# Optimization experiments

Measured on AMD Instinct MI355X. Metric: run time of the kernel, lower is better.

The kernel has to match this reference:

```python
import jax, jax.numpy as jnp
import numpy as np

N = 50000          # nodes
E = 800000         # edges (avg degree 16)
DIN = 128          # d_input
H = 8              # heads per layer
D = 16             # per-head hidden dim
HID = H * D        # 128
ALPHA = 0.2        # LeakyReLU negative slope in GAT attention
BN_EPS = 1e-5


def _xavier(key, shape):
    fan_in, fan_out = shape[0], shape[-1]
    lim = np.sqrt(6.0 / (fan_in + fan_out)).astype(np.float32)
    return jax.random.uniform(key, shape, jnp.float32, -lim, lim)


def setup_inputs() -> dict:
    key = jax.random.key(0)
    ks = jax.random.split(key, 8)
    x = jax.random.normal(ks[0], (N, DIN), jnp.float32)
    edge_idx = jax.random.randint(ks[1], (2, E), 0, N)
    W1 = _xavier(ks[2], (DIN, HID))
    a1 = _xavier(ks[3], (H, 2 * D))
    W2 = _xavier(ks[4], (HID, HID))
    a2 = _xavier(ks[5], (H, 2 * D))
    W3 = _xavier(ks[6], (HID, HID))
    a3 = _xavier(ks[7], (H, 2 * D))
    ones = jnp.ones((HID,), jnp.float32)
    zeros = jnp.zeros((HID,), jnp.float32)
    return {"x": x, "edge_idx": edge_idx,
            "W1": W1, "a1": a1, "W2": W2, "a2": a2, "W3": W3, "a3": a3,
            "g1": ones, "b1": zeros, "g2": ones, "b2": zeros, "g3": ones, "b3": zeros}


def _leaky(x):
    return jnp.where(x >= 0, x, ALPHA * x)


def _gat_layer(x, src, dst, W, a):
    # x: [N, Fin]; W: [Fin, H*D]; a: [H, 2D]
    h = (x @ W).reshape(-1, H, D)                       # [N, H, D]
    e_src = jnp.einsum('nhd,hd->nh', h, a[:, :D])       # a^T part for source node
    e_dst = jnp.einsum('nhd,hd->nh', h, a[:, D:])       # a^T part for destination node
    e = _leaky(e_src[src] + e_dst[dst])                 # [E, H]
    m = jax.ops.segment_max(e, dst, num_segments=N)     # per-dst stable softmax max
    m = jnp.where(jnp.isfinite(m), m, 0.0)              # empty segments -> 0
    w = jnp.exp(e - m[dst])                             # [E, H]
    den = jax.ops.segment_sum(w, dst, num_segments=N)   # [N, H]
    agg = jax.ops.segment_sum(h[src] * w[:, :, None], dst, num_segments=N)  # [N, H, D]
    out = agg / (den[:, :, None] + 1e-16)
    return out.reshape(-1, HID)                         # concat heads


def _bn(x, g, b):
    # BatchNorm1d training-mode math over the node axis
    mu = x.mean(axis=0)
    var = x.var(axis=0)
    return g * (x - mu) * jax.lax.rsqrt(var + BN_EPS) + b


def reference(x, edge_idx, W1, a1, W2, a2, W3, a3, g1, b1, g2, b2, g3, b3):
    src, dst = edge_idx[0], edge_idx[1]
    h1 = jax.nn.elu(_bn(_gat_layer(x, src, dst, W1, a1), g1, b1))
    h2 = jax.nn.elu(_bn(_gat_layer(h1, src, dst, W2, a2), g2, b2))
    h3_in = h1 + h2  # skip connection
    return _bn(_gat_layer(h3_in, src, dst, W3, a3), g3, b3)
```

## Files before the change

kernel.cpp:

```cpp
#include <hip/hip_runtime.h>
#include <hip/hip_bf16.h>
#include <hip/hip_fp16.h>
#include <cstddef>

#define NNODES 50000
#define NEDGES 800000
#define HID 128
#define NHEAD 8
#define AGG_NB (NNODES / 16)
#define NSLICE 64
#define SLAYER (NSLICE * 512)

#define NBUCK 196
#define BCH 2048
#define BIN_NB ((NEDGES + BCH - 1) / BCH)

typedef __attribute__((ext_vector_type(4))) float floatx4;
typedef _Float16 __attribute__((ext_vector_type(8))) half8;
typedef _Float16 __attribute__((ext_vector_type(2))) half2v;

static inline size_t align_up(size_t x, size_t a) { return (x + a - 1) & ~(a - 1); }

__device__ inline float fexp2(float x) {
#if __has_builtin(__builtin_amdgcn_exp2f)
    return __builtin_amdgcn_exp2f(x);
#else
    return __expf(x * 0.69314718055994531f);
#endif
}

__device__ inline unsigned short f2h(float f) {
    return __builtin_bit_cast(unsigned short, (_Float16)f);
}

__global__ __launch_bounds__(256) void init_kernel(const float* __restrict__ W1,
                                                   const float* __restrict__ W2,
                                                   const float* __restrict__ W3,
                                                   unsigned short* __restrict__ Wt,
                                                   int* __restrict__ zeroA, int nA,
                                                   float* __restrict__ zeroB, int nB) {
    int b = blockIdx.x;
    int t = threadIdx.x;
    if (b < 192) {
        int layer = b >> 6;
        const float* W = (layer == 0) ? W1 : ((layer == 1) ? W2 : W3);
        int idx = (b & 63) * 256 + t;
        int n = idx & 127;
        int k = idx >> 7;
        Wt[layer * 16384 + n * 128 + k] = f2h(W[idx]);
    } else {
        int nb = gridDim.x - 192;
        int bb = b - 192;
        for (int i = bb * 256 + t; i < nA; i += nb * 256) zeroA[i] = 0;
        for (int i = bb * 256 + t; i < nB; i += nb * 256) zeroB[i] = 0.f;
    }
}

__global__ __launch_bounds__(256) void bin_count_kernel(const int* __restrict__ edge,
                                                        int* __restrict__ bucketCnt) {
    __shared__ int h[NBUCK];
    int t = threadIdx.x;
    if (t < NBUCK) h[t] = 0;
    __syncthreads();
    for (int i = blockIdx.x * 256 + t; i < NEDGES; i += gridDim.x * 256)
        atomicAdd(&h[edge[NEDGES + i] >> 8], 1);
    __syncthreads();
    if (t < NBUCK && h[t]) atomicAdd(&bucketCnt[t], h[t]);
}

__global__ __launch_bounds__(256) void bucket_scan_kernel(const int* __restrict__ bucketCnt,
                                                          int* __restrict__ bucketBase) {
    __shared__ int sA[256];
    int t = threadIdx.x;
    int v = (t < NBUCK) ? bucketCnt[t] : 0;
    sA[t] = v;
    __syncthreads();
    for (int off = 1; off < 256; off <<= 1) {
        int x = (t >= off) ? sA[t - off] : 0;
        __syncthreads();
        sA[t] += x;
        __syncthreads();
    }
    if (t < NBUCK) bucketBase[t] = sA[t] - v;
    if (t == 0) bucketBase[NBUCK] = NEDGES;
}

__global__ __launch_bounds__(256) void bin_scatter_kernel(const int* __restrict__ edge,
                                                          const int* __restrict__ bucketBase,
                                                          int* __restrict__ bucketCursor,
                                                          unsigned int* __restrict__ binned) {
    __shared__ int sA[256];
    __shared__ int hcnt[NBUCK];
    __shared__ int hbase[NBUCK];
    __shared__ int gbase[NBUCK];
    __shared__ unsigned int sEnt[BCH];
    __shared__ unsigned char sBk[BCH];
    int t = threadIdx.x;
    int e0 = blockIdx.x * BCH;
    int nv = NEDGES - e0;
    if (nv > BCH) nv = BCH;

    if (t < NBUCK) hcnt[t] = 0;
    __syncthreads();

    int myB[8];
    int myR[8];
    unsigned int myP[8];
    #pragma unroll
    for (int j = 0; j < 8; ++j) {
        int idx = j * 256 + t;
        myB[j] = -1;
        if (idx < nv) {
            int s = edge[e0 + idx];
            int d = edge[NEDGES + e0 + idx];
            int bk = d >> 8;
            myB[j] = bk;
            myP[j] = (unsigned)s | ((unsigned)(d & 255) << 16);
            myR[j] = atomicAdd(&hcnt[bk], 1);
        }
    }
    __syncthreads();
    int hc = (t < NBUCK) ? hcnt[t] : 0;
    sA[t] = hc;
    __syncthreads();
    for (int off = 1; off < 256; off <<= 1) {
        int x = (t >= off) ? sA[t - off] : 0;
        __syncthreads();
        sA[t] += x;
        __syncthreads();
    }
    if (t < NBUCK) {
        hbase[t] = sA[t] - hc;
        gbase[t] = bucketBase[t] + atomicAdd(&bucketCursor[t], hc);
    }
    __syncthreads();
    #pragma unroll
    for (int j = 0; j < 8; ++j) {
        if (myB[j] >= 0) {
            int p = hbase[myB[j]] + myR[j];
            sEnt[p] = myP[j];
            sBk[p] = (unsigned char)myB[j];
        }
    }
    __syncthreads();
    #pragma unroll
    for (int j = 0; j < 8; ++j) {
        int i = j * 256 + t;
        if (i < nv) {
            int bk = sBk[i];
            binned[gbase[bk] + (i - hbase[bk])] = sEnt[i];
        }
    }
}

__global__ __launch_bounds__(256) void fine_csr_kernel(const int* __restrict__ bucketCnt,
                                                       const int* __restrict__ bucketBase,
                                                       const unsigned int* __restrict__ binned,
                                                       int* __restrict__ offs,
                                                       int* __restrict__ csr) {
    __shared__ int sA[256];
    __shared__ int sB[256];
    int t = threadIdx.x;
    int b = blockIdx.x;
    int cntb = bucketCnt[b];
    int base = bucketBase[b];
    sB[t] = 0;
    __syncthreads();
    for (int i = t; i < cntb; i += 256)
        atomicAdd(&sB[(binned[base + i] >> 16) & 255], 1);
    __syncthreads();
    int nc = sB[t];
    sA[t] = nc;
    __syncthreads();
    for (int off = 1; off < 256; off <<= 1) {
        int x = (t >= off) ? sA[t - off] : 0;
        __syncthreads();
        sA[t] += x;
        __syncthreads();
    }
    int nodeBase = base + sA[t] - nc;
    int gid = b * 256 + t;
    if (gid < NNODES) offs[gid] = nodeBase;
    if (b == NBUCK - 1 && t == 0) offs[NNODES] = NEDGES;
    sB[t] = nodeBase;
    __syncthreads();
    for (int i = t; i < cntb; i += 256) {
        unsigned e = binned[base + i];
        int pos = atomicAdd(&sB[(e >> 16) & 255], 1);
        csr[pos] = (int)(e & 0xFFFFu);
    }
}

__global__ __launch_bounds__(256) void bn_finalize_kernel(const float* __restrict__ statsPart,
                                                          const float* __restrict__ g,
                                                          const float* __restrict__ b,
                                                          float* __restrict__ ssv) {
    __shared__ float sm[256];
    int t = threadIdx.x;
    const float* base = statsPart + (t & 127) + ((t >> 7) << 7);
    float s = 0.f;
    #pragma unroll 8
    for (int k = 0; k < NSLICE; ++k) s += base[k * 512];
    sm[t] = s;
    __syncthreads();
    if (t < 128) {
        float mu = sm[t] / (float)NNODES;
        float var = sm[128 + t] / (float)NNODES - mu * mu;
        float rstd = rsqrtf(var + 1e-5f);
        float scale = g[t] * rstd;
        ssv[t] = scale;
        ssv[128 + t] = b[t] - mu * scale;
    }
}

#define GROWS 32
#define TSTRIDE 76
#define LOG2E 1.4426950408889634f
__global__ __launch_bounds__(256, 4) void gemm_kernel(const float* __restrict__ Xin,
                                                      const float* __restrict__ skip,
                                                      const float* __restrict__ ssv,
                                                      const unsigned short* __restrict__ Wt,
                                                      const float* __restrict__ a,
                                                      float* __restrict__ Hw,
                                                      unsigned short* __restrict__ Hb,
                                                      float* __restrict__ esrc,
                                                      float* __restrict__ edst,
                                                      int mode) {
    __shared__ unsigned short As[4 * 16 * TSTRIDE];
    int tid = threadIdx.x;
    int wv = tid >> 6;
    int lane = tid & 63;
    int l15 = lane & 15;
    int quad = lane >> 4;
    int whalf = wv & 1;
    int rowBase = blockIdx.x * GROWS + (wv >> 1) * 16;
    int gr = rowBase + l15;
    bool valid = gr < NNODES;

    float4 va[8];
    if (valid) {
        const float* xr = Xin + (size_t)gr * HID + quad * 8;
        #pragma unroll
        for (int c = 0; c < 4; ++c) {
            va[2 * c]     = *(const float4*)(xr + c * 32);
            va[2 * c + 1] = *(const float4*)(xr + c * 32 + 4);
        }
    } else {
        #pragma unroll
        for (int j = 0; j < 8; ++j) va[j] = make_float4(0.f, 0.f, 0.f, 0.f);
    }
    float4 vs[8];
    if (mode == 2 && valid) {
        const float* sr = skip + (size_t)gr * HID + quad * 8;
        #pragma unroll
        for (int c = 0; c < 4; ++c) {
            vs[2 * c]     = *(const float4*)(sr + c * 32);
            vs[2 * c + 1] = *(const float4*)(sr + c * 32 + 4);
        }
    }

    half8 bf[2][4];
    {
        const unsigned short* wb = Wt + ((whalf * 4) * 16 + l15) * 128 + quad * 8;
        #pragma unroll
        for (int c = 0; c < 4; ++c) bf[0][c] = *(const half8*)(wb + c * 32);
    }

    if (mode >= 1 && valid) {
        #pragma unroll
        for (int c = 0; c < 4; ++c) {
            #pragma unroll
            for (int hh = 0; hh < 2; ++hh) {
                int ch = quad * 8 + c * 32 + hh * 4;
                float4 sc = *(const float4*)(ssv + ch);
                float4 sh = *(const float4*)(ssv + 128 + ch);
                float4 v = va[2 * c + hh];
                v.x = sc.x * v.x + sh.x;
                v.y = sc.y * v.y + sh.y;
                v.z = sc.z * v.z + sh.z;
                v.w = sc.w * v.w + sh.w;
                v.x = (v.x > 0.f) ? v.x : expm1f(v.x);
                v.y = (v.y > 0.f) ? v.y : expm1f(v.y);
                v.z = (v.z > 0.f) ? v.z : expm1f(v.z);
                v.w = (v.w > 0.f) ? v.w : expm1f(v.w);
                if (mode == 2) {
                    float4 s = vs[2 * c + hh];
                    v.x += s.x; v.y += s.y; v.z += s.z; v.w += s.w;
                }
                va[2 * c + hh] = v;
            }
        }
        if (mode == 1 && whalf == 0) {
            float* hw = Hw + (size_t)gr * HID + quad * 8;
            #pragma unroll
            for (int c = 0; c < 4; ++c) {
                *(float4*)(hw + c * 32)     = va[2 * c];
                *(float4*)(hw + c * 32 + 4) = va[2 * c + 1];
            }
        }
    }
    half8 af[4];
    #pragma unroll
    for (int c = 0; c < 4; ++c) {
        uint4 pk;
        pk.x = __builtin_bit_cast(unsigned int, __builtin_amdgcn_cvt_pkrtz(va[2*c].x,   va[2*c].y));
        pk.y = __builtin_bit_cast(unsigned int, __builtin_amdgcn_cvt_pkrtz(va[2*c].z,   va[2*c].w));
        pk.z = __builtin_bit_cast(unsigned int, __builtin_amdgcn_cvt_pkrtz(va[2*c+1].x, va[2*c+1].y));
        pk.w = __builtin_bit_cast(unsigned int, __builtin_amdgcn_cvt_pkrtz(va[2*c+1].z, va[2*c+1].w));
        af[c] = __builtin_bit_cast(half8, pk);
    }

    floatx4 acc[4];
    #pragma unroll
    for (int hb = 0; hb < 4; ++hb) {
        if (hb < 3) {
            const unsigned short* wn = Wt + ((whalf * 4 + hb + 1) * 16 + l15) * 128 + quad * 8;
            #pragma unroll
            for (int c = 0; c < 4; ++c) bf[(hb + 1) & 1][c] = *(const half8*)(wn + c * 32);
        }
        acc[hb] = (floatx4){0.f, 0.f, 0.f, 0.f};
        #pragma unroll
        for (int c = 0; c < 4; ++c)
            acc[hb] = __builtin_amdgcn_mfma_f32_16x16x32_f16(af[c], bf[hb & 1][c], acc[hb], 0, 0, 0);
    }

    unsigned short* ws = &As[wv * 16 * TSTRIDE];
    #pragma unroll
    for (int hb = 0; hb < 4; ++hb) {
        #pragma unroll
        for (int reg = 0; reg < 4; ++reg)
            ws[(quad * 4 + reg) * TSTRIDE + hb * 16 + l15] = f2h(acc[hb][reg]);
    }

    {
        int rloc = lane >> 2;
        int cpart = lane & 3;
        int grow = rowBase + rloc;
        const unsigned short* rrow = &ws[rloc * TSTRIDE + cpart * 16];
        uint4 u0 = *(const uint4*)(rrow);
        uint4 u1 = *(const uint4*)(rrow + 8);
        if (grow < NNODES) {
            int chb = whalf * 64 + cpart * 16;
            uint4* dst = (uint4*)(Hb + (size_t)grow * HID + chb);
            dst[0] = u0;
            dst[1] = u1;
            float f[16];
            {
                unsigned int* pu = (unsigned int*)&u0;
                #pragma unroll
                for (int j = 0; j < 4; ++j) {
                    half2v hv = __builtin_bit_cast(half2v, pu[j]);
                    f[2 * j]     = (float)hv[0];
                    f[2 * j + 1] = (float)hv[1];
                }
                pu = (unsigned int*)&u1;
                #pragma unroll
                for (int j = 0; j < 4; ++j) {
                    half2v hv = __builtin_bit_cast(half2v, pu[j]);
                    f[8 + 2 * j]     = (float)hv[0];
                    f[8 + 2 * j + 1] = (float)hv[1];
                }
            }
            int head = whalf * 4 + cpart;
            float es = 0.f, ev = 0.f;
            #pragma unroll
            for (int j = 0; j < 16; ++j) {
                es += f[j] * a[head * 32 + j];
                ev += f[j] * a[head * 32 + 16 + j];
            }
            esrc[grow * NHEAD + head] = es * LOG2E;
            edst[grow * NHEAD + head] = ev * LOG2E;
        }
    }
}

__global__ __launch_bounds__(256) void aggregate_kernel(const int* __restrict__ offs,
                                                        const int* __restrict__ csr,
                                                        const float* __restrict__ esrc,
                                                        const float* __restrict__ edst,
                                                        const unsigned int* __restrict__ Hb,
                                                        float* __restrict__ out,
                                                        float* __restrict__ statsPart) {
    int tid = threadIdx.x;
    int wv = tid >> 6;
    int lane = tid & 63;
    int grp = lane >> 4;
    int sub = lane & 15;
    int head = sub >> 1;
    int n = blockIdx.x * 16 + wv * 4 + grp;
    int beg = offs[n], end = offs[n + 1];
    float ed = edst[n * NHEAD + head];
    float acc[8];
    #pragma unroll
    for (int q = 0; q < 8; ++q) acc[q] = 0.f;
    float den = 0.f;
    for (int i = beg; i < end; i += 4) {
        int ss[4];
        #pragma unroll
        for (int j = 0; j < 4; ++j)
            ss[j] = csr[min(i + j, end - 1)];
        float ee[4];
        uint4 hh[4];
        #pragma unroll
        for (int j = 0; j < 4; ++j)
            ee[j] = esrc[(unsigned)ss[j] * 8u + (unsigned)head];
        #pragma unroll
        for (int j = 0; j < 4; ++j)
            hh[j] = *(const uint4*)(Hb + (unsigned)ss[j] * 64u + (unsigned)sub * 4u);
        #pragma unroll
        for (int j = 0; j < 4; ++j) {
            float e = ee[j] + ed;
            e = fmaxf(e, 0.2f * e);
            float w = fexp2(e);
            w = (i + j < end) ? w : 0.f;
            den += w;
            half2v h0 = __builtin_bit_cast(half2v, hh[j].x);
            half2v h1 = __builtin_bit_cast(half2v, hh[j].y);
            half2v h2 = __builtin_bit_cast(half2v, hh[j].z);
            half2v h3 = __builtin_bit_cast(half2v, hh[j].w);
            acc[0] += w * (float)h0[0];
            acc[1] += w * (float)h0[1];
            acc[2] += w * (float)h1[0];
            acc[3] += w * (float)h1[1];
            acc[4] += w * (float)h2[0];
            acc[5] += w * (float)h2[1];
            acc[6] += w * (float)h3[0];
            acc[7] += w * (float)h3[1];
        }
    }
    float inv = 1.f / (den + 1e-16f);
    float4 o0 = make_float4(acc[0] * inv, acc[1] * inv, acc[2] * inv, acc[3] * inv);
    float4 o1 = make_float4(acc[4] * inv, acc[5] * inv, acc[6] * inv, acc[7] * inv);
    float* orow = out + (size_t)n * HID + sub * 8;
    *(float4*)orow = o0;
    *(float4*)(orow + 4) = o1;

    __shared__ float sm[16 * 136];
    float* srow = &sm[(wv * 4 + grp) * 136 + sub * 8];
    *(float4*)srow = o0;
    *(float4*)(srow + 4) = o1;
    __syncthreads();
    if (tid < 128) {
        float s = 0.f, s2 = 0.f;
        #pragma unroll
        for (int rr = 0; rr < 16; ++rr) {
            float v = sm[rr * 136 + tid];
            s += v;
            s2 += v * v;
        }
        float* slice = statsPart + (blockIdx.x & (NSLICE - 1)) * 512;
        atomicAdd(&slice[tid], s);
        atomicAdd(&slice[128 + tid], s2);
    }
}

__global__ __launch_bounds__(256) void final_apply_kernel(const float* __restrict__ X,
                                                          const float* __restrict__ ssv,
                                                          float* __restrict__ out) {
    __shared__ float ssm[256];
    int tid = threadIdx.x;
    ssm[tid] = ssv[tid];
    __syncthreads();
    int total4 = NNODES * HID / 4;
    for (int i = blockIdx.x * 256 + tid; i < total4; i += gridDim.x * 256) {
        float4 v = ((const float4*)X)[i];
        int c4 = (i & 31) * 4;
        float4 sc = *(const float4*)(ssm + c4);
        float4 sh = *(const float4*)(ssm + 128 + c4);
        v.x = sc.x * v.x + sh.x;
        v.y = sc.y * v.y + sh.y;
        v.z = sc.z * v.z + sh.z;
        v.w = sc.w * v.w + sh.w;
        ((float4*)out)[i] = v;
    }
}

extern "C" void kernel_launch(void* const* d_in, const int* in_sizes, int n_in,
                              void* d_out, int out_size, void* d_ws, size_t ws_size,
                              hipStream_t stream) {
    const float* x   = (const float*)d_in[0];
    const int* edge  = (const int*)d_in[1];
    const float* W1  = (const float*)d_in[2];
    const float* a1  = (const float*)d_in[3];
    const float* W2  = (const float*)d_in[4];
    const float* a2  = (const float*)d_in[5];
    const float* W3  = (const float*)d_in[6];
    const float* a3  = (const float*)d_in[7];
    const float* g1  = (const float*)d_in[8];
    const float* b1  = (const float*)d_in[9];
    const float* g2  = (const float*)d_in[10];
    const float* b2  = (const float*)d_in[11];
    const float* g3  = (const float*)d_in[12];
    const float* b3  = (const float*)d_in[13];
    float* outp      = (float*)d_out;

    char* p = (char*)d_ws;
    size_t cur = 0;
    auto carve = [&](size_t bytes) {
        void* r = p + cur;
        cur = align_up(cur + bytes, 256);
        return r;
    };
    int*   offs   = (int*)carve((NNODES + 1) * sizeof(int));
    int*   csr    = (int*)carve(NEDGES * sizeof(int));
    unsigned short* wt = (unsigned short*)carve(3 * 16384 * sizeof(unsigned short));
    unsigned short* hb = (unsigned short*)carve((size_t)NNODES * HID * sizeof(unsigned short));
    float* agg    = (float*)carve((size_t)NNODES * HID * sizeof(float));
    float* h1     = (float*)carve((size_t)NNODES * HID * sizeof(float));
    float* esrc   = (float*)carve((size_t)NNODES * NHEAD * sizeof(float));
    float* edst   = (float*)carve((size_t)NNODES * NHEAD * sizeof(float));
    float* stats  = (float*)carve(3 * SLAYER * sizeof(float));
    int*   bcnt   = (int*)carve((3 * NBUCK + 1) * sizeof(int));
    int*   bcur   = bcnt + NBUCK;
    int*   bbase  = bcnt + 2 * NBUCK;
    float* ssv    = (float*)carve(3 * 256 * sizeof(float));
    float* stats1 = stats;
    float* stats2 = stats + SLAYER;
    float* stats3 = stats + 2 * SLAYER;
    float* ssv1 = ssv;
    float* ssv2 = ssv + 256;
    float* ssv3 = ssv + 512;
    unsigned int* binned = (unsigned int*)h1;

    const int GB = (NNODES + GROWS - 1) / GROWS;

    init_kernel<<<256, 256, 0, stream>>>(W1, W2, W3, wt,
                                         bcnt, 2 * NBUCK,
                                         stats, 3 * SLAYER);
    bin_count_kernel<<<256, 256, 0, stream>>>(edge, bcnt);
    bucket_scan_kernel<<<1, 256, 0, stream>>>(bcnt, bbase);
    bin_scatter_kernel<<<BIN_NB, 256, 0, stream>>>(edge, bbase, bcur, binned);
    fine_csr_kernel<<<NBUCK, 256, 0, stream>>>(bcnt, bbase, binned, offs, csr);

    gemm_kernel<<<GB, 256, 0, stream>>>(x, nullptr, nullptr,
                                        wt, a1, nullptr, hb, esrc, edst, 0);
    aggregate_kernel<<<AGG_NB, 256, 0, stream>>>(offs, csr, esrc, edst,
                                                 (const unsigned int*)hb, agg, stats1);
    bn_finalize_kernel<<<1, 256, 0, stream>>>(stats1, g1, b1, ssv1);

    gemm_kernel<<<GB, 256, 0, stream>>>(agg, nullptr, ssv1,
                                        wt + 16384, a2, h1, hb, esrc, edst, 1);
    aggregate_kernel<<<AGG_NB, 256, 0, stream>>>(offs, csr, esrc, edst,
                                                 (const unsigned int*)hb, agg, stats2);
    bn_finalize_kernel<<<1, 256, 0, stream>>>(stats2, g2, b2, ssv2);

    gemm_kernel<<<GB, 256, 0, stream>>>(agg, h1, ssv2,
                                        wt + 32768, a3, nullptr, hb, esrc, edst, 2);
    aggregate_kernel<<<AGG_NB, 256, 0, stream>>>(offs, csr, esrc, edst,
                                                 (const unsigned int*)hb, agg, stats3);
    bn_finalize_kernel<<<1, 256, 0, stream>>>(stats3, g3, b3, ssv3);

    final_apply_kernel<<<768, 256, 0, stream>>>(agg, ssv3, outp);
}
```

Measured before the change: 395.2 us.

## Split GEMM block by column quarters to cut registers and raise occupancy

The GEMM kernel now handles 16 rows per block, with each of the four waves computing 32 output columns (two heads) instead of 64 columns over 32 rows. This shrinks per-thread accumulator and weight-fragment registers, drops the double-buffered weight prefetch, and raises the launch-bounds occupancy hint from 4 to 6 blocks. The skip input is now loaded inline rather than prefetched. In exchange, each input row is loaded and BN/ELU-transformed by all four waves instead of two, which adds redundant global loads and ALU work, and only half the lanes compute the attention scores.

```diff
diff --git a/kernel.cpp b/kernel.cpp
--- a/kernel.cpp
+++ b/kernel.cpp
@@ -213,10 +213,10 @@
     }
 }
 
-#define GROWS 32
-#define TSTRIDE 76
+#define GROWS 16
+#define TSTRIDE 40
 #define LOG2E 1.4426950408889634f
-__global__ __launch_bounds__(256, 4) void gemm_kernel(const float* __restrict__ Xin,
+__global__ __launch_bounds__(256, 6) void gemm_kernel(const float* __restrict__ Xin,
                                                       const float* __restrict__ skip,
                                                       const float* __restrict__ ssv,
                                                       const unsigned short* __restrict__ Wt,
@@ -232,8 +232,7 @@
     int lane = tid & 63;
     int l15 = lane & 15;
     int quad = lane >> 4;
-    int whalf = wv & 1;
-    int rowBase = blockIdx.x * GROWS + (wv >> 1) * 16;
+    int rowBase = blockIdx.x * GROWS;
     int gr = rowBase + l15;
     bool valid = gr < NNODES;
 
@@ -249,21 +248,11 @@
         #pragma unroll
         for (int j = 0; j < 8; ++j) va[j] = make_float4(0.f, 0.f, 0.f, 0.f);
     }
-    float4 vs[8];
-    if (mode == 2 && valid) {
-        const float* sr = skip + (size_t)gr * HID + quad * 8;
-        #pragma unroll
-        for (int c = 0; c < 4; ++c) {
-            vs[2 * c]     = *(const float4*)(sr + c * 32);
-            vs[2 * c + 1] = *(const float4*)(sr + c * 32 + 4);
-        }
-    }
-
-    half8 bf[2][4];
+    half8 bf0[4];
     {
-        const unsigned short* wb = Wt + ((whalf * 4) * 16 + l15) * 128 + quad * 8;
-        #pragma unroll
-        for (int c = 0; c < 4; ++c) bf[0][c] = *(const half8*)(wb + c * 32);
+        const unsigned short* wb = Wt + ((2 * wv) * 16 + l15) * 128 + quad * 8;
+        #pragma unroll
+        for (int c = 0; c < 4; ++c) bf0[c] = *(const half8*)(wb + c * 32);
     }
 
     if (mode >= 1 && valid) {
@@ -284,13 +273,14 @@
                 v.z = (v.z > 0.f) ? v.z : expm1f(v.z);
                 v.w = (v.w > 0.f) ? v.w : expm1f(v.w);
                 if (mode == 2) {
-                    float4 s = vs[2 * c + hh];
+                    const float* sr = skip + (size_t)gr * HID + ch;
+                    float4 s = *(const float4*)sr;
                     v.x += s.x; v.y += s.y; v.z += s.z; v.w += s.w;
                 }
                 va[2 * c + hh] = v;
             }
         }
-        if (mode == 1 && whalf == 0) {
+        if (mode == 1 && wv == 0) {
             float* hw = Hw + (size_t)gr * HID + quad * 8;
             #pragma unroll
             for (int c = 0; c < 4; ++c) {
@@ -310,58 +300,61 @@
         af[c] = __builtin_bit_cast(half8, pk);
     }
 
-    floatx4 acc[4];
-    #pragma unroll
-    for (int hb = 0; hb < 4; ++hb) {
-        if (hb < 3) {
-            const unsigned short* wn = Wt + ((whalf * 4 + hb + 1) * 16 + l15) * 128 + quad * 8;
-            #pragma unroll
-            for (int c = 0; c < 4; ++c) bf[(hb + 1) & 1][c] = *(const half8*)(wn + c * 32);
-        }
-        acc[hb] = (floatx4){0.f, 0.f, 0.f, 0.f};
-        #pragma unroll
-        for (int c = 0; c < 4; ++c)
-            acc[hb] = __builtin_amdgcn_mfma_f32_16x16x32_f16(af[c], bf[hb & 1][c], acc[hb], 0, 0, 0);
-    }
+    half8 bf1[4];
+    {
+        const unsigned short* wb = Wt + ((2 * wv + 1) * 16 + l15) * 128 + quad * 8;
+        #pragma unroll
+        for (int c = 0; c < 4; ++c) bf1[c] = *(const half8*)(wb + c * 32);
+    }
+    floatx4 acc0 = (floatx4){0.f, 0.f, 0.f, 0.f};
+    floatx4 acc1 = (floatx4){0.f, 0.f, 0.f, 0.f};
+    #pragma unroll
+    for (int c = 0; c < 4; ++c)
+        acc0 = __builtin_amdgcn_mfma_f32_16x16x32_f16(af[c], bf0[c], acc0, 0, 0, 0);
+    #pragma unroll
+    for (int c = 0; c < 4; ++c)
+        acc1 = __builtin_amdgcn_mfma_f32_16x16x32_f16(af[c], bf1[c], acc1, 0, 0, 0);
 
     unsigned short* ws = &As[wv * 16 * TSTRIDE];
     #pragma unroll
-    for (int hb = 0; hb < 4; ++hb) {
-        #pragma unroll
-        for (int reg = 0; reg < 4; ++reg)
-            ws[(quad * 4 + reg) * TSTRIDE + hb * 16 + l15] = f2h(acc[hb][reg]);
+    for (int reg = 0; reg < 4; ++reg) {
+        ws[(quad * 4 + reg) * TSTRIDE + l15]      = f2h(acc0[reg]);
+        ws[(quad * 4 + reg) * TSTRIDE + 16 + l15] = f2h(acc1[reg]);
     }
 
     {
         int rloc = lane >> 2;
-        int cpart = lane & 3;
+        int seg = lane & 3;
         int grow = rowBase + rloc;
-        const unsigned short* rrow = &ws[rloc * TSTRIDE + cpart * 16];
+        uint4 u = *(const uint4*)(&ws[rloc * TSTRIDE + seg * 8]);
+        if (grow < NNODES)
+            *(uint4*)(Hb + (size_t)grow * HID + wv * 32 + seg * 8) = u;
+    }
+
+    if (lane < 32) {
+        int rloc = lane >> 1;
+        int lb = lane & 1;
+        int grow = rowBase + rloc;
+        const unsigned short* rrow = &ws[rloc * TSTRIDE + lb * 16];
         uint4 u0 = *(const uint4*)(rrow);
         uint4 u1 = *(const uint4*)(rrow + 8);
         if (grow < NNODES) {
-            int chb = whalf * 64 + cpart * 16;
-            uint4* dst = (uint4*)(Hb + (size_t)grow * HID + chb);
-            dst[0] = u0;
-            dst[1] = u1;
             float f[16];
-            {
-                unsigned int* pu = (unsigned int*)&u0;
-                #pragma unroll
-                for (int j = 0; j < 4; ++j) {
-                    half2v hv = __builtin_bit_cast(half2v, pu[j]);
-                    f[2 * j]     = (float)hv[0];
-                    f[2 * j + 1] = (float)hv[1];
-                }
-                pu = (unsigned int*)&u1;
-                #pragma unroll
-                for (int j = 0; j < 4; ++j) {
-                    half2v hv = __builtin_bit_cast(half2v, pu[j]);
-                    f[8 + 2 * j]     = (float)hv[0];
-                    f[8 + 2 * j + 1] = (float)hv[1];
-                }
+            unsigned int* pu = (unsigned int*)&u0;
+            #pragma unroll
+            for (int j = 0; j < 4; ++j) {
+                half2v hv = __builtin_bit_cast(half2v, pu[j]);
+                f[2 * j]     = (float)hv[0];
+                f[2 * j + 1] = (float)hv[1];
             }
-            int head = whalf * 4 + cpart;
+            pu = (unsigned int*)&u1;
+            #pragma unroll
+            for (int j = 0; j < 4; ++j) {
+                half2v hv = __builtin_bit_cast(half2v, pu[j]);
+                f[8 + 2 * j]     = (float)hv[0];
+                f[8 + 2 * j + 1] = (float)hv[1];
+            }
+            int head = wv * 2 + lb;
             float es = 0.f, ev = 0.f;
             #pragma unroll
             for (int j = 0; j < 16; ++j) {
```

Result: slower. 431.6 us (+9.2%).
